# Performance work log

Hardware: AMD Instinct MI355X
Metric: run time of the kernel (lower is better)

## Reference

```python
import jax, jax.numpy as jnp
from jax import lax
import numpy as np

CHUNK = 64      # chunk_size init kwarg
MAX_LOG = 20.0  # clamp bound used in ssd()
DT_BIAS = 0.01
NEG_SLOPE = 0.01  # torch LeakyReLU default


def segsum(a):
    """a: (..., T) -> (..., T, T); ss[i,j] = sum_{k=j+1..i} a[k], -inf above diag."""
    T = a.shape[-1]
    rep = jnp.broadcast_to(a[..., :, None], a.shape + (T,))
    strict_lower = jnp.tril(jnp.ones((T, T), dtype=bool), -1)
    ss = jnp.cumsum(jnp.where(strict_lower, rep, 0.0), axis=-2)
    keep = jnp.tril(jnp.ones((T, T), dtype=bool), 0)
    return jnp.where(keep, ss, -jnp.inf)


def setup_inputs() -> dict:
    key = jax.random.key(0)
    ks = jax.random.split(key, 7)
    T, B, S, F = 4096, 4, 16, 64   # time, batch, spatial heads, in_channels
    N, P, K = 16, 64, 5            # state_dim, head_dim, conv_size
    CH = 2 * N + P + 1             # bc_conv out channels = 97
    return {
        "x": jax.random.normal(ks[0], (T, B, S, F), dtype=jnp.float32),
        "conv_w": jax.random.normal(ks[1], (CH, F, K), dtype=jnp.float32) * 0.05,
        "conv_b": jax.random.normal(ks[2], (CH,), dtype=jnp.float32) * 0.05,
        "pass_w": jax.random.normal(ks[3], (1, F), dtype=jnp.float32) * 0.1,
        "pass_b": jax.random.normal(ks[4], (1,), dtype=jnp.float32) * 0.1,
        "red_w": jax.random.normal(ks[5], (1, P), dtype=jnp.float32) * 0.1,
        "red_b": jax.random.normal(ks[6], (1,), dtype=jnp.float32) * 0.1,
        "dt_param": jnp.zeros((1,), dtype=jnp.float32),  # torch init [0.0]
    }


def _forward(x, conv_w, conv_b, pass_w, pass_b, red_w, red_b, dt_param):
    T, B, S, F = x.shape
    CH, _, K = conv_w.shape
    P = red_w.shape[1]
    N = (CH - P - 1) // 2
    c = T // CHUNK

    # ---- _compute_ssm_params (parallel mode, causal left-pad) ----
    xr = jnp.moveaxis(x.reshape(T, B * S, F), 0, 2)          # (bs, F, T)
    xp = jnp.pad(xr, ((0, 0), (0, 0), (K - 1, 0)))           # left pad context
    bcax = lax.conv_general_dilated(
        xp, conv_w, window_strides=(1,), padding="VALID",
        dimension_numbers=("NCH", "OIH", "NCH")) + conv_b[None, :, None]
    bcax = jax.nn.sigmoid(bcax) + bcax                        # (bs, CH, T)
    bcax = bcax.reshape(B, S, CH, T)
    Bm = bcax[:, :, :N, :]                                    # (b,s,n,t)
    Cm = bcax[:, :, N:2 * N, :]                               # (b,s,n,t)
    A = -jnp.abs(bcax[:, :, 2 * N, :])                        # (b,s,t)
    Xc = bcax[:, :, 2 * N + 1:, :]                            # (b,s,p,t)
    dt = jax.nn.softplus(dt_param)[0] + DT_BIAS
    lAd = dt * A                                              # (b,s,t)
    Bd = Bm * ((jnp.exp(lAd) - 1.0) / (A + 1e-9))[:, :, None, :]
    Dx = x @ pass_w[0] + pass_b[0]                            # (t,b,s) passthrough

    # ---- ssd: chunked Mamba-2 scan ----
    Xb = jnp.moveaxis(Xc, 3, 0).swapaxes(0, 1).reshape(B, c, CHUNK, S, P)
    Bb = jnp.moveaxis(Bd, 3, 0).swapaxes(0, 1).reshape(B, c, CHUNK, S, N)
    Cb = jnp.moveaxis(Cm, 3, 0).swapaxes(0, 1).reshape(B, c, CHUNK, S, N)
    Ab = lAd.reshape(B, S, c, CHUNK)                          # (b,s,c,l)
    A_cumsum = jnp.cumsum(Ab, axis=-1)                        # (b,s,c,l)

    L = jnp.exp(jnp.clip(segsum(Ab), -MAX_LOG, MAX_LOG))      # (b,s,c,l,l)
    Y_diag = jnp.einsum("bclsn,bcmsn,bsclm,bcmsp->bclsp", Cb, Bb, L, Xb)

    decay_states = jnp.exp(jnp.clip(A_cumsum[..., -1:] - A_cumsum, -MAX_LOG, MAX_LOG))
    states = jnp.einsum("bclsn,bscl,bclsp->bcspn", Bb, decay_states, Xb)
    states = jnp.concatenate([jnp.zeros_like(states[:, :1]), states], axis=1)

    A_last = jnp.pad(A_cumsum[..., -1], ((0, 0), (0, 0), (1, 0)))  # (b,s,c+1)
    decay_chunk = jnp.exp(jnp.clip(segsum(A_last), -MAX_LOG, MAX_LOG))
    new_states = jnp.einsum("bszc,bcspn->bzspn", decay_chunk, states)
    states_c = new_states[:, :-1]                             # (b,c,s,p,n)

    state_decay_out = jnp.exp(A_cumsum)                       # (b,s,c,l), no clamp (as in source)
    Y_off = jnp.einsum("bclsn,bcspn,bscl->bclsp", Cb, states_c, state_decay_out)

    Y = (Y_diag + Y_off).reshape(B, T, S, P).swapaxes(0, 1)   # (t,b,s,p)

    # ---- reduce + leaky-relu passthrough ----
    y = Y @ red_w[0] + red_b[0]                               # (t,b,s)
    return y + jnp.where(Dx >= 0, Dx, NEG_SLOPE * Dx)


def reference(x, conv_w, conv_b, pass_w, pass_b, red_w, red_b, dt_param):
    return _forward(x, conv_w, conv_b, pass_w, pass_b, red_w, red_b, dt_param)
```

## Files before the change

### kernel.cpp

```cpp
#include <hip/hip_runtime.h>
#include <hip/hip_bf16.h>
#include <math.h>


#define Tn 4096
#define BSn 64
#define Fn 64
#define CHn 97
#define CHP 112
#define Kn 5
#define Nn 16
#define NCn 64

typedef __attribute__((ext_vector_type(8))) short bf16x8;
typedef __attribute__((ext_vector_type(4))) float f32x4;

static __device__ __forceinline__ unsigned short f2bf(float v) {
    __hip_bfloat16 b = __float2bfloat16(v);
    return *reinterpret_cast<unsigned short*>(&b);
}
static __device__ __forceinline__ float bf2f(unsigned short u) {
    unsigned v = ((unsigned)u) << 16;
    return __builtin_bit_cast(float, v);
}

#define OFF_BD   0
#define OFF_CM   (OFF_BD + 4194304)
#define OFF_LAD  (OFF_CM + 4194304)
#define OFF_XQ   (OFF_LAD + 262144)
#define OFF_DL   (OFF_XQ + 262144)
#define OFF_ACS  (OFF_DL + 262144)
#define OFF_SRED (OFF_ACS + 262144)
#define OFF_CSUM (OFF_SRED + 65536)
#define OFF_SNS  (OFF_CSUM + 4096)
#define OFF_WBH  (OFF_SNS + 65536)
#define OFF_WBL  (OFF_WBH + 17920)

__global__ __launch_bounds__(256) void k_prep(const float* __restrict__ conv_w,
                                              const float* __restrict__ pass_w,
                                              unsigned short* __restrict__ wbh,
                                              unsigned short* __restrict__ wbl) {
    int idx = blockIdx.x * 256 + threadIdx.x;
    if (idx >= Kn * CHP * Fn) return;
    int f = idx & 63;
    int rest = idx >> 6;
    int ch = rest % CHP;
    int k = rest / CHP;
    float w = 0.f;
    if (ch < CHn) w = conv_w[(ch * Fn + f) * Kn + k];
    else if (ch == 97 && k == 4) w = pass_w[f];
    unsigned short hi = f2bf(w);
    wbh[idx] = hi;
    if (ch >= 32 && ch < 48)
        wbl[(k * 16 + (ch - 32)) * 64 + f] = f2bf(w - bf2f(hi));
}

__global__ __launch_bounds__(256) void k_conv(
    const float* __restrict__ x, const unsigned short* __restrict__ wbh,
    const unsigned short* __restrict__ wbl,
    const float* __restrict__ conv_b, const float* __restrict__ pass_b,
    const float* __restrict__ red_w, const float* __restrict__ red_b,
    const float* __restrict__ dtp,
    float* __restrict__ Bd_t, float* __restrict__ Cm_t,
    float* __restrict__ lAd_ws, float* __restrict__ xq_ws,
    float* __restrict__ DL_ws) {
    const int ci = blockIdx.x, bs = blockIdx.y;
    const int tid = threadIdx.x;
    const int wv = tid >> 6, lane = tid & 63;
    const int qd = lane >> 4, n = lane & 15;

    __shared__ alignas(16) unsigned short xsb[68 * 72];
    __shared__ alignas(16) unsigned short xlo[68 * 72];
    __shared__ float zsh[64];
    __shared__ float pxl[4][64];

    const int tB = (wv == 3) ? 6 : wv + 4;
    const unsigned short* pBw = (wv == 2) ? wbl : wbh;
    const int sB = (wv == 2) ? 16 : CHP;
    const int cB = (wv == 2) ? 0 : 16 * tB;
    bf16x8 wA[10], wB[10];
#pragma unroll
    for (int s = 0; s < 10; ++s) {
        const int k = s >> 1, f0 = 32 * (s & 1) + qd * 8;
        wA[s] = *(const bf16x8*)&wbh[((k * CHP + 16 * wv + n) << 6) + f0];
        wB[s] = *(const bf16x8*)&pBw[((k * sB + cB + n) << 6) + f0];
    }

    float4 v[5];
#pragma unroll
    for (int it = 0; it < 5; ++it) {
        int idx = tid + it * 256;
        int tt = idx >> 4, fq = (idx & 15) * 4;
        int t = ci * 64 - 4 + tt;
        v[it] = (idx < 68 * 16 && t >= 0)
                    ? *(const float4*)&x[(t * 64 + bs) * 64 + fq]
                    : make_float4(0.f, 0.f, 0.f, 0.f);
    }
#pragma unroll
    for (int it = 0; it < 5; ++it) {
        int idx = tid + it * 256;
        if (idx < 68 * 16) {
            int tt = idx >> 4, fq = (idx & 15) * 4;
            ushort4 h, lo;
            h.x = f2bf(v[it].x); lo.x = f2bf(v[it].x - bf2f(h.x));
            h.y = f2bf(v[it].y); lo.y = f2bf(v[it].y - bf2f(h.y));
            h.z = f2bf(v[it].z); lo.z = f2bf(v[it].z - bf2f(h.z));
            h.w = f2bf(v[it].w); lo.w = f2bf(v[it].w - bf2f(h.w));
            *(ushort4*)&xsb[tt * 72 + fq] = h;
            *(ushort4*)&xlo[tt * 72 + fq] = lo;
        }
    }
    __syncthreads();

    f32x4 accA[4], accB[4];
#pragma unroll
    for (int rg = 0; rg < 4; ++rg) {
        accA[rg] = (f32x4){0.f, 0.f, 0.f, 0.f};
        accB[rg] = (f32x4){0.f, 0.f, 0.f, 0.f};
    }
    if (wv == 2) {
#pragma unroll
        for (int s = 0; s < 10; ++s) {
            const int k = s >> 1, f0 = 32 * (s & 1) + qd * 8;
#pragma unroll
            for (int rg = 0; rg < 4; ++rg) {
                bf16x8 av = *(const bf16x8*)&xsb[(16 * rg + n + k) * 72 + f0];
                bf16x8 al = *(const bf16x8*)&xlo[(16 * rg + n + k) * 72 + f0];
                accA[rg] = __builtin_amdgcn_mfma_f32_16x16x32_bf16(av, wA[s], accA[rg], 0, 0, 0);
                accA[rg] = __builtin_amdgcn_mfma_f32_16x16x32_bf16(al, wA[s], accA[rg], 0, 0, 0);
                accA[rg] = __builtin_amdgcn_mfma_f32_16x16x32_bf16(av, wB[s], accA[rg], 0, 0, 0);
            }
        }
    } else {
#pragma unroll
        for (int s = 0; s < 10; ++s) {
            const int k = s >> 1, f0 = 32 * (s & 1) + qd * 8;
#pragma unroll
            for (int rg = 0; rg < 4; ++rg) {
                bf16x8 av = *(const bf16x8*)&xsb[(16 * rg + n + k) * 72 + f0];
                accA[rg] = __builtin_amdgcn_mfma_f32_16x16x32_bf16(av, wA[s], accA[rg], 0, 0, 0);
                accB[rg] = __builtin_amdgcn_mfma_f32_16x16x32_bf16(av, wB[s], accB[rg], 0, 0, 0);
            }
        }
    }

    const int cbase = (bs * 64 + ci) * 64;
    float px[4][4];
#pragma unroll
    for (int rg = 0; rg < 4; ++rg)
#pragma unroll
        for (int reg = 0; reg < 4; ++reg) px[rg][reg] = 0.f;

    if (wv == 0) {
        const float cb4 = conv_b[64 + n], rw4 = red_w[31 + n];
#pragma unroll
        for (int rg = 0; rg < 4; ++rg)
#pragma unroll
            for (int reg = 0; reg < 4; ++reg) {
                float z = accB[rg][reg] + cb4;
                px[rg][reg] = (z + 1.f / (1.f + __expf(-z))) * rw4;
            }
    } else if (wv == 1) {
        const float cb1 = conv_b[16 + n];
        const float cb5 = conv_b[80 + n], rw5 = red_w[47 + n];
#pragma unroll
        for (int rg = 0; rg < 4; ++rg)
#pragma unroll
            for (int reg = 0; reg < 4; ++reg) {
                float z1 = accA[rg][reg] + cb1;
                Cm_t[(cbase + 16 * rg + 4 * qd + reg) * 16 + n] =
                    z1 + 1.f / (1.f + __expf(-z1));
                float z5 = accB[rg][reg] + cb5;
                px[rg][reg] = (z5 + 1.f / (1.f + __expf(-z5))) * rw5;
            }
    } else if (wv == 2) {
        const float cb2 = conv_b[32 + n];
        const float rw2 = (n >= 1) ? red_w[n - 1] : 0.f;
#pragma unroll
        for (int rg = 0; rg < 4; ++rg)
#pragma unroll
            for (int reg = 0; reg < 4; ++reg) {
                if (n == 0) zsh[16 * rg + 4 * qd + reg] = accA[rg][reg];
                float z = accA[rg][reg] + cb2;
                px[rg][reg] = (z + 1.f / (1.f + __expf(-z))) * rw2;
            }
    } else {
        const float cb3 = conv_b[48 + n], rw3 = red_w[15 + n];
        const float cb6 = conv_b[96], rw6 = red_w[63];
        const float pb = pass_b[0], rb = red_b[0];
#pragma unroll
        for (int rg = 0; rg < 4; ++rg)
#pragma unroll
            for (int reg = 0; reg < 4; ++reg) {
                float z3 = accA[rg][reg] + cb3;
                px[rg][reg] = (z3 + 1.f / (1.f + __expf(-z3))) * rw3;
                if (n == 0) {
                    float z6 = accB[rg][reg] + cb6;
                    px[rg][reg] += (z6 + 1.f / (1.f + __expf(-z6))) * rw6;
                }
                if (n == 1) {
                    float Dx = accB[rg][reg] + pb;
                    float DL = (Dx >= 0.f) ? Dx : 0.01f * Dx;
                    DL_ws[bs * Tn + ci * 64 + 16 * rg + 4 * qd + reg] = DL + rb;
                }
            }
    }

#pragma unroll
    for (int m = 1; m < 16; m <<= 1)
#pragma unroll
        for (int rg = 0; rg < 4; ++rg)
#pragma unroll
            for (int reg = 0; reg < 4; ++reg)
                px[rg][reg] += __shfl_xor(px[rg][reg], m, 64);
    if (n == 0)
#pragma unroll
        for (int rg = 0; rg < 4; ++rg)
#pragma unroll
            for (int reg = 0; reg < 4; ++reg)
                pxl[wv][16 * rg + 4 * qd + reg] = px[rg][reg];
    __syncthreads();

    if (wv == 0) {
        const float dt = log1pf(expf(dtp[0])) + 0.01f;
        float zA = zsh[lane] + conv_b[32];
        float aA = zA + 1.f / (1.f + __expf(-zA));
        float An = -fabsf(aA);
        float lAd = dt * An;
        lAd_ws[bs * Tn + ci * 64 + lane] = lAd;
        float fl = (__expf(lAd) - 1.f) / (An + 1e-9f);
        const float cb0 = conv_b[n];
#pragma unroll
        for (int rg = 0; rg < 4; ++rg)
#pragma unroll
            for (int reg = 0; reg < 4; ++reg) {
                float z = accA[rg][reg] + cb0;
                float a = z + 1.f / (1.f + __expf(-z));
                float fr = __shfl(fl, 16 * rg + 4 * qd + reg, 64);
                Bd_t[(cbase + 16 * rg + 4 * qd + reg) * 16 + n] = a * fr;
            }
    } else if (wv == 1) {
        xq_ws[bs * Tn + ci * 64 + lane] =
            pxl[0][lane] + pxl[1][lane] + pxl[2][lane] + pxl[3][lane];
    }
}

__global__ __launch_bounds__(256) void k_chunk(
    const float* __restrict__ lAd_ws, const float* __restrict__ xq_ws,
    const float* __restrict__ Bd_t, float* __restrict__ Acs_ws,
    float* __restrict__ sred_ws, float* __restrict__ csum_ws) {
    const int bs = blockIdx.y;
    const int tid = threadIdx.x, wv = tid >> 6, l = tid & 63;
    const int ci = blockIdx.x * 4 + wv;
    __shared__ float aL[4][64], acs[4][64], vv[4][64];
    __shared__ float Bt[4][64 * 17], part[4][4][16];
    const int base = bs * Tn + ci * 64;

    aL[wv][l] = lAd_ws[base + l];
    const float4* brow = (const float4*)&Bd_t[((bs * 64 + ci) * 64 + l) * 16];
    float4 b0 = brow[0], b1 = brow[1], b2 = brow[2], b3 = brow[3];
    float* bt = &Bt[wv][l * 17];
    bt[0] = b0.x;  bt[1] = b0.y;  bt[2] = b0.z;  bt[3] = b0.w;
    bt[4] = b1.x;  bt[5] = b1.y;  bt[6] = b1.z;  bt[7] = b1.w;
    bt[8] = b2.x;  bt[9] = b2.y;  bt[10] = b2.z; bt[11] = b2.w;
    bt[12] = b3.x; bt[13] = b3.y; bt[14] = b3.z; bt[15] = b3.w;
    __syncthreads();

    float s = 0.f;
    for (int k2 = 0; k2 < 64; ++k2) {
        float a = aL[wv][k2];
        if (k2 <= l) s += a;
    }
    acs[wv][l] = s;
    Acs_ws[base + l] = s;
    __syncthreads();

    float tot = acs[wv][63];
    float ds = __expf(fmaxf(tot - s, -20.f));
    vv[wv][l] = ds * xq_ws[base + l];
    __syncthreads();

    int nn = l & 15, q = l >> 4;
    float p = 0.f;
#pragma unroll
    for (int i = 0; i < 16; ++i)
        p += Bt[wv][(q * 16 + i) * 17 + nn] * vv[wv][q * 16 + i];
    part[wv][q][nn] = p;
    __syncthreads();
    if (l < 16)
        sred_ws[(bs * 64 + ci) * 16 + l] =
            part[wv][0][l] + part[wv][1][l] + part[wv][2][l] + part[wv][3][l];
    if (l == 0) csum_ws[bs * 64 + ci] = tot;
}

__global__ __launch_bounds__(256) void k_scan(const float* __restrict__ sred_ws,
                                              const float* __restrict__ csum_ws,
                                              float* __restrict__ sns_ws) {
    const int wid = blockIdx.x * 4 + (threadIdx.x >> 6);
    const int ci = threadIdx.x & 63;
    const int bs = wid >> 4, n = wid & 15;
    float s = sred_ws[(bs * 64 + ci) * 16 + n];
    float d = __expf(csum_ws[bs * 64 + ci]);
#pragma unroll
    for (int k = 1; k < 64; k <<= 1) {
        float dp = __shfl_up(d, k, 64);
        float sp = __shfl_up(s, k, 64);
        if (ci >= k) {
            s = d * sp + s;
            d = d * dp;
        }
    }
    float se = __shfl_up(s, 1, 64);
    sns_ws[(bs * 64 + ci) * 16 + n] = (ci == 0) ? 0.f : se;
}

__global__ __launch_bounds__(256) void k_y(
    const float* __restrict__ Cm_t, const float* __restrict__ Bd_t,
    const float* __restrict__ xq_ws, const float* __restrict__ Acs_ws,
    const float* __restrict__ sns_ws, const float* __restrict__ DL_ws,
    float* __restrict__ out) {
    const int bs = blockIdx.y;
    const int tid = threadIdx.x;
    const int wv = tid >> 6, l = tid & 63;
    const int ci = blockIdx.x * 4 + wv;
    __shared__ float Bt[4][64 * 17], xv[4][64], ac[4][64], sn[4][16];
    const int base = bs * Tn + ci * 64;

    xv[wv][l] = xq_ws[base + l];
    ac[wv][l] = Acs_ws[base + l];
    if (l < 16) sn[wv][l] = sns_ws[(bs * 64 + ci) * 16 + l];
    const float4* brow = (const float4*)&Bd_t[((bs * 64 + ci) * 64 + l) * 16];
    float4 b0 = brow[0], b1 = brow[1], b2 = brow[2], b3 = brow[3];
    float* bt = &Bt[wv][l * 17];
    bt[0] = b0.x;  bt[1] = b0.y;  bt[2] = b0.z;  bt[3] = b0.w;
    bt[4] = b1.x;  bt[5] = b1.y;  bt[6] = b1.z;  bt[7] = b1.w;
    bt[8] = b2.x;  bt[9] = b2.y;  bt[10] = b2.z; bt[11] = b2.w;
    bt[12] = b3.x; bt[13] = b3.y; bt[14] = b3.z; bt[15] = b3.w;
    const float4* crow = (const float4*)&Cm_t[((bs * 64 + ci) * 64 + l) * 16];
    float4 c0 = crow[0], c1 = crow[1], c2 = crow[2], c3 = crow[3];
    __syncthreads();

    const float acl = ac[wv][l];
    float y = 0.f;
    for (int m = 0; m < 64; ++m) {
        const float* br = &Bt[wv][m * 17];
        float g = c0.x * br[0] + c0.y * br[1] + c0.z * br[2] + c0.w * br[3] +
                  c1.x * br[4] + c1.y * br[5] + c1.z * br[6] + c1.w * br[7] +
                  c2.x * br[8] + c2.y * br[9] + c2.z * br[10] + c2.w * br[11] +
                  c3.x * br[12] + c3.y * br[13] + c3.z * br[14] + c3.w * br[15];
        float arg = (m <= l) ? fmaxf(acl - ac[wv][m], -20.f) : -20.f;
        y += __expf(arg) * g * xv[wv][m];
    }
    const float* s = sn[wv];
    float go = c0.x * s[0] + c0.y * s[1] + c0.z * s[2] + c0.w * s[3] +
               c1.x * s[4] + c1.y * s[5] + c1.z * s[6] + c1.w * s[7] +
               c2.x * s[8] + c2.y * s[9] + c2.z * s[10] + c2.w * s[11] +
               c3.x * s[12] + c3.y * s[13] + c3.z * s[14] + c3.w * s[15];
    y += __expf(acl) * go;

    out[(ci * 64 + l) * 64 + bs] = y + DL_ws[base + l];
}

extern "C" void kernel_launch(void* const* d_in, const int* in_sizes, int n_in,
                              void* d_out, int out_size, void* d_ws,
                              size_t ws_size, hipStream_t stream) {
    const float* x = (const float*)d_in[0];
    const float* conv_w = (const float*)d_in[1];
    const float* conv_b = (const float*)d_in[2];
    const float* pass_w = (const float*)d_in[3];
    const float* pass_b = (const float*)d_in[4];
    const float* red_w = (const float*)d_in[5];
    const float* red_b = (const float*)d_in[6];
    const float* dtp = (const float*)d_in[7];
    float* out = (float*)d_out;
    float* W = (float*)d_ws;
    (void)in_sizes; (void)n_in; (void)out_size; (void)ws_size;

    float* Bd_t = W + OFF_BD;
    float* Cm_t = W + OFF_CM;
    float* lAd_ws = W + OFF_LAD;
    float* xq_ws = W + OFF_XQ;
    float* DL_ws = W + OFF_DL;
    float* Acs_ws = W + OFF_ACS;
    float* sred_ws = W + OFF_SRED;
    float* csum_ws = W + OFF_CSUM;
    float* sns_ws = W + OFF_SNS;
    unsigned short* wbh = (unsigned short*)(W + OFF_WBH);
    unsigned short* wbl = (unsigned short*)(W + OFF_WBL);

    k_prep<<<dim3((Kn * CHP * Fn + 255) / 256), dim3(256), 0, stream>>>(
        conv_w, pass_w, wbh, wbl);
    k_conv<<<dim3(NCn, BSn), dim3(256), 0, stream>>>(
        x, wbh, wbl, conv_b, pass_b, red_w, red_b, dtp,
        Bd_t, Cm_t, lAd_ws, xq_ws, DL_ws);
    k_chunk<<<dim3(NCn / 4, BSn), dim3(256), 0, stream>>>(
        lAd_ws, xq_ws, Bd_t, Acs_ws, sred_ws, csum_ws);
    k_scan<<<dim3(256), dim3(256), 0, stream>>>(sred_ws, csum_ws, sns_ws);
    k_y<<<dim3(NCn / 4, BSn), dim3(256), 0, stream>>>(
        Cm_t, Bd_t, xq_ws, Acs_ws, sns_ws, DL_ws, out);
}
```

Before: 200.3 us.

## Fuse chunk-local state and diagonal output into conv kernel, drop Bd round-trip

Merges the chunk-local work (within-chunk cumsum of log decay, chunk state reduction, and intra-chunk diagonal output) into the conv kernel. B, C and the per-chunk scalars stay in a reused shared-memory pool instead of going to global memory and being re-read by two later kernels. The final kernel now only adds the inter-chunk state contribution to a precomputed partial output. This removes one launch and the Bd_t/lAd/xq/DL global traffic, at the cost of a longer conv kernel with extra barriers and more per-block LDS and register pressure.

```diff
diff --git a/kernel.cpp b/kernel.cpp
--- a/kernel.cpp
+++ b/kernel.cpp
@@ -55,24 +55,29 @@
         wbl[(k * 16 + (ch - 32)) * 64 + f] = f2bf(w - bf2f(hi));
 }
 
-__global__ __launch_bounds__(256) void k_conv(
+__global__ __launch_bounds__(256) void k_fwd(
     const float* __restrict__ x, const unsigned short* __restrict__ wbh,
     const unsigned short* __restrict__ wbl,
     const float* __restrict__ conv_b, const float* __restrict__ pass_b,
     const float* __restrict__ red_w, const float* __restrict__ red_b,
     const float* __restrict__ dtp,
-    float* __restrict__ Bd_t, float* __restrict__ Cm_t,
-    float* __restrict__ lAd_ws, float* __restrict__ xq_ws,
-    float* __restrict__ DL_ws) {
+    float* __restrict__ Cm_t, float* __restrict__ Acs_ws,
+    float* __restrict__ yp_ws, float* __restrict__ sred_ws,
+    float* __restrict__ csum_ws) {
     const int ci = blockIdx.x, bs = blockIdx.y;
     const int tid = threadIdx.x;
     const int wv = tid >> 6, lane = tid & 63;
     const int qd = lane >> 4, n = lane & 15;
 
-    __shared__ alignas(16) unsigned short xsb[68 * 72];
-    __shared__ alignas(16) unsigned short xlo[68 * 72];
-    __shared__ float zsh[64];
-    __shared__ float pxl[4][64];
+    __shared__ alignas(16) unsigned char pool[19584];
+    unsigned short* xsb = (unsigned short*)pool;
+    unsigned short* xlo = (unsigned short*)(pool + 9792);
+    float* B0  = (float*)pool;
+    float* Ct  = (float*)(pool + 5120);
+    float* pxl = (float*)(pool + 10240);
+    float* px2 = (float*)(pool + 11264);
+    float* zsh = (float*)(pool + 12288);
+    float* dl  = (float*)(pool + 12544);
 
     const int tB = (wv == 3) ? 6 : wv + 4;
     const unsigned short* pBw = (wv == 2) ? wbl : wbh;
@@ -143,6 +148,7 @@
             }
         }
     }
+    __syncthreads();
 
     const int cbase = (bs * 64 + ci) * 64;
     float px[4][4];
@@ -152,13 +158,19 @@
         for (int reg = 0; reg < 4; ++reg) px[rg][reg] = 0.f;
 
     if (wv == 0) {
+        const float cb0 = conv_b[n];
         const float cb4 = conv_b[64 + n], rw4 = red_w[31 + n];
 #pragma unroll
         for (int rg = 0; rg < 4; ++rg)
 #pragma unroll
             for (int reg = 0; reg < 4; ++reg) {
-                float z = accB[rg][reg] + cb4;
-                px[rg][reg] = (z + 1.f / (1.f + __expf(-z))) * rw4;
+                int row = 16 * rg + 4 * qd + reg;
+                float z0 = accA[rg][reg] + cb0;
+                float a0 = z0 + 1.f / (1.f + __expf(-z0));
+                accA[rg][reg] = a0;
+                B0[row * 20 + n] = a0;
+                float z4 = accB[rg][reg] + cb4;
+                px[rg][reg] = (z4 + 1.f / (1.f + __expf(-z4))) * rw4;
             }
     } else if (wv == 1) {
         const float cb1 = conv_b[16 + n];
@@ -167,9 +179,11 @@
         for (int rg = 0; rg < 4; ++rg)
 #pragma unroll
             for (int reg = 0; reg < 4; ++reg) {
+                int row = 16 * rg + 4 * qd + reg;
                 float z1 = accA[rg][reg] + cb1;
-                Cm_t[(cbase + 16 * rg + 4 * qd + reg) * 16 + n] =
-                    z1 + 1.f / (1.f + __expf(-z1));
+                float a1 = z1 + 1.f / (1.f + __expf(-z1));
+                Ct[row * 20 + n] = a1;
+                Cm_t[(cbase + row) * 16 + n] = a1;
                 float z5 = accB[rg][reg] + cb5;
                 px[rg][reg] = (z5 + 1.f / (1.f + __expf(-z5))) * rw5;
             }
@@ -180,7 +194,8 @@
         for (int rg = 0; rg < 4; ++rg)
 #pragma unroll
             for (int reg = 0; reg < 4; ++reg) {
-                if (n == 0) zsh[16 * rg + 4 * qd + reg] = accA[rg][reg];
+                int row = 16 * rg + 4 * qd + reg;
+                if (n == 0) zsh[row] = accA[rg][reg];
                 float z = accA[rg][reg] + cb2;
                 px[rg][reg] = (z + 1.f / (1.f + __expf(-z))) * rw2;
             }
@@ -192,6 +207,7 @@
         for (int rg = 0; rg < 4; ++rg)
 #pragma unroll
             for (int reg = 0; reg < 4; ++reg) {
+                int row = 16 * rg + 4 * qd + reg;
                 float z3 = accA[rg][reg] + cb3;
                 px[rg][reg] = (z3 + 1.f / (1.f + __expf(-z3))) * rw3;
                 if (n == 0) {
@@ -201,11 +217,10 @@
                 if (n == 1) {
                     float Dx = accB[rg][reg] + pb;
                     float DL = (Dx >= 0.f) ? Dx : 0.01f * Dx;
-                    DL_ws[bs * Tn + ci * 64 + 16 * rg + 4 * qd + reg] = DL + rb;
+                    dl[row] = DL + rb;
                 }
             }
     }
-
 #pragma unroll
     for (int m = 1; m < 16; m <<= 1)
 #pragma unroll
@@ -218,79 +233,71 @@
         for (int rg = 0; rg < 4; ++rg)
 #pragma unroll
             for (int reg = 0; reg < 4; ++reg)
-                pxl[wv][16 * rg + 4 * qd + reg] = px[rg][reg];
-    __syncthreads();
+                pxl[wv * 64 + 16 * rg + 4 * qd + reg] = px[rg][reg];
+    __syncthreads();
+
+    const int l = lane;
+    const float dt = log1pf(expf(dtp[0])) + 0.01f;
+    float zA = zsh[l] + conv_b[32];
+    float aA = zA + 1.f / (1.f + __expf(-zA));
+    float An = -fabsf(aA);
+    float lAd = dt * An;
+    float fac = (__expf(lAd) - 1.f) / (An + 1e-9f);
+    float s = lAd;
+#pragma unroll
+    for (int k = 1; k < 64; k <<= 1) {
+        float t = __shfl_up(s, k, 64);
+        if (l >= k) s += t;
+    }
+    const float acs_l = s;
+    const float tot = __shfl(s, 63, 64);
+    float xq = pxl[0 * 64 + l] + pxl[1 * 64 + l] + pxl[2 * 64 + l] + pxl[3 * 64 + l];
+    const float wd = fac * xq;
+    const float wsd = wd * __expf(fmaxf(tot - acs_l, -20.f));
+    if (wv == 3) {
+        Acs_ws[bs * Tn + ci * 64 + l] = acs_l;
+        if (l == 0) csum_ws[bs * 64 + ci] = tot;
+    }
+
+    const float4 cc0 = *(const float4*)&Ct[l * 20 + 0];
+    const float4 cc1 = *(const float4*)&Ct[l * 20 + 4];
+    const float4 cc2 = *(const float4*)&Ct[l * 20 + 8];
+    const float4 cc3 = *(const float4*)&Ct[l * 20 + 12];
+    float part = 0.f;
+#pragma unroll
+    for (int mm = 0; mm < 16; ++mm) {
+        const int m = 16 * wv + mm;
+        const float4 b0 = *(const float4*)&B0[m * 20 + 0];
+        const float4 b1 = *(const float4*)&B0[m * 20 + 4];
+        const float4 b2 = *(const float4*)&B0[m * 20 + 8];
+        const float4 b3 = *(const float4*)&B0[m * 20 + 12];
+        float g = cc0.x * b0.x + cc0.y * b0.y + cc0.z * b0.z + cc0.w * b0.w +
+                  cc1.x * b1.x + cc1.y * b1.y + cc1.z * b1.z + cc1.w * b1.w +
+                  cc2.x * b2.x + cc2.y * b2.y + cc2.z * b2.z + cc2.w * b2.w +
+                  cc3.x * b3.x + cc3.y * b3.y + cc3.z * b3.z + cc3.w * b3.w;
+        float am = __shfl(acs_l, m, 64);
+        float wm = __shfl(wd, m, 64);
+        float arg = (m <= l) ? fmaxf(acs_l - am, -20.f) : -20.f;
+        part += __expf(arg) * g * wm;
+    }
+    px2[wv * 64 + l] = part;
 
     if (wv == 0) {
-        const float dt = log1pf(expf(dtp[0])) + 0.01f;
-        float zA = zsh[lane] + conv_b[32];
-        float aA = zA + 1.f / (1.f + __expf(-zA));
-        float An = -fabsf(aA);
-        float lAd = dt * An;
-        lAd_ws[bs * Tn + ci * 64 + lane] = lAd;
-        float fl = (__expf(lAd) - 1.f) / (An + 1e-9f);
-        const float cb0 = conv_b[n];
-#pragma unroll
-        for (int rg = 0; rg < 4; ++rg)
-#pragma unroll
-            for (int reg = 0; reg < 4; ++reg) {
-                float z = accA[rg][reg] + cb0;
-                float a = z + 1.f / (1.f + __expf(-z));
-                float fr = __shfl(fl, 16 * rg + 4 * qd + reg, 64);
-                Bd_t[(cbase + 16 * rg + 4 * qd + reg) * 16 + n] = a * fr;
-            }
-    } else if (wv == 1) {
-        xq_ws[bs * Tn + ci * 64 + lane] =
-            pxl[0][lane] + pxl[1][lane] + pxl[2][lane] + pxl[3][lane];
-    }
-}
-
-__global__ __launch_bounds__(256) void k_chunk(
-    const float* __restrict__ lAd_ws, const float* __restrict__ xq_ws,
-    const float* __restrict__ Bd_t, float* __restrict__ Acs_ws,
-    float* __restrict__ sred_ws, float* __restrict__ csum_ws) {
-    const int bs = blockIdx.y;
-    const int tid = threadIdx.x, wv = tid >> 6, l = tid & 63;
-    const int ci = blockIdx.x * 4 + wv;
-    __shared__ float aL[4][64], acs[4][64], vv[4][64];
-    __shared__ float Bt[4][64 * 17], part[4][4][16];
-    const int base = bs * Tn + ci * 64;
-
-    aL[wv][l] = lAd_ws[base + l];
-    const float4* brow = (const float4*)&Bd_t[((bs * 64 + ci) * 64 + l) * 16];
-    float4 b0 = brow[0], b1 = brow[1], b2 = brow[2], b3 = brow[3];
-    float* bt = &Bt[wv][l * 17];
-    bt[0] = b0.x;  bt[1] = b0.y;  bt[2] = b0.z;  bt[3] = b0.w;
-    bt[4] = b1.x;  bt[5] = b1.y;  bt[6] = b1.z;  bt[7] = b1.w;
-    bt[8] = b2.x;  bt[9] = b2.y;  bt[10] = b2.z; bt[11] = b2.w;
-    bt[12] = b3.x; bt[13] = b3.y; bt[14] = b3.z; bt[15] = b3.w;
-    __syncthreads();
-
-    float s = 0.f;
-    for (int k2 = 0; k2 < 64; ++k2) {
-        float a = aL[wv][k2];
-        if (k2 <= l) s += a;
-    }
-    acs[wv][l] = s;
-    Acs_ws[base + l] = s;
-    __syncthreads();
-
-    float tot = acs[wv][63];
-    float ds = __expf(fmaxf(tot - s, -20.f));
-    vv[wv][l] = ds * xq_ws[base + l];
-    __syncthreads();
-
-    int nn = l & 15, q = l >> 4;
-    float p = 0.f;
-#pragma unroll
-    for (int i = 0; i < 16; ++i)
-        p += Bt[wv][(q * 16 + i) * 17 + nn] * vv[wv][q * 16 + i];
-    part[wv][q][nn] = p;
-    __syncthreads();
-    if (l < 16)
-        sred_ws[(bs * 64 + ci) * 16 + l] =
-            part[wv][0][l] + part[wv][1][l] + part[wv][2][l] + part[wv][3][l];
-    if (l == 0) csum_ws[bs * 64 + ci] = tot;
+        float sp = 0.f;
+#pragma unroll
+        for (int rg = 0; rg < 4; ++rg)
+#pragma unroll
+            for (int reg = 0; reg < 4; ++reg)
+                sp += accA[rg][reg] * __shfl(wsd, 16 * rg + 4 * qd + reg, 64);
+        sp += __shfl_xor(sp, 16, 64);
+        sp += __shfl_xor(sp, 32, 64);
+        if (l < 16) sred_ws[(bs * 64 + ci) * 16 + l] = sp;
+    }
+    __syncthreads();
+
+    if (wv == 0)
+        yp_ws[bs * Tn + ci * 64 + l] =
+            px2[0 * 64 + l] + px2[1 * 64 + l] + px2[2 * 64 + l] + px2[3 * 64 + l] + dl[l];
 }
 
 __global__ __launch_bounds__(256) void k_scan(const float* __restrict__ sred_ws,
@@ -314,51 +321,30 @@
     sns_ws[(bs * 64 + ci) * 16 + n] = (ci == 0) ? 0.f : se;
 }
 
-__global__ __launch_bounds__(256) void k_y(
-    const float* __restrict__ Cm_t, const float* __restrict__ Bd_t,
-    const float* __restrict__ xq_ws, const float* __restrict__ Acs_ws,
-    const float* __restrict__ sns_ws, const float* __restrict__ DL_ws,
+__global__ __launch_bounds__(256) void k_out(
+    const float* __restrict__ Cm_t, const float* __restrict__ Acs_ws,
+    const float* __restrict__ sns_ws, const float* __restrict__ yp_ws,
     float* __restrict__ out) {
     const int bs = blockIdx.y;
     const int tid = threadIdx.x;
     const int wv = tid >> 6, l = tid & 63;
     const int ci = blockIdx.x * 4 + wv;
-    __shared__ float Bt[4][64 * 17], xv[4][64], ac[4][64], sn[4][16];
+    __shared__ float sn[4][16];
     const int base = bs * Tn + ci * 64;
 
-    xv[wv][l] = xq_ws[base + l];
-    ac[wv][l] = Acs_ws[base + l];
     if (l < 16) sn[wv][l] = sns_ws[(bs * 64 + ci) * 16 + l];
-    const float4* brow = (const float4*)&Bd_t[((bs * 64 + ci) * 64 + l) * 16];
-    float4 b0 = brow[0], b1 = brow[1], b2 = brow[2], b3 = brow[3];
-    float* bt = &Bt[wv][l * 17];
-    bt[0] = b0.x;  bt[1] = b0.y;  bt[2] = b0.z;  bt[3] = b0.w;
-    bt[4] = b1.x;  bt[5] = b1.y;  bt[6] = b1.z;  bt[7] = b1.w;
-    bt[8] = b2.x;  bt[9] = b2.y;  bt[10] = b2.z; bt[11] = b2.w;
-    bt[12] = b3.x; bt[13] = b3.y; bt[14] = b3.z; bt[15] = b3.w;
     const float4* crow = (const float4*)&Cm_t[((bs * 64 + ci) * 64 + l) * 16];
     float4 c0 = crow[0], c1 = crow[1], c2 = crow[2], c3 = crow[3];
-    __syncthreads();
-
-    const float acl = ac[wv][l];
-    float y = 0.f;
-    for (int m = 0; m < 64; ++m) {
-        const float* br = &Bt[wv][m * 17];
-        float g = c0.x * br[0] + c0.y * br[1] + c0.z * br[2] + c0.w * br[3] +
-                  c1.x * br[4] + c1.y * br[5] + c1.z * br[6] + c1.w * br[7] +
-                  c2.x * br[8] + c2.y * br[9] + c2.z * br[10] + c2.w * br[11] +
-                  c3.x * br[12] + c3.y * br[13] + c3.z * br[14] + c3.w * br[15];
-        float arg = (m <= l) ? fmaxf(acl - ac[wv][m], -20.f) : -20.f;
-        y += __expf(arg) * g * xv[wv][m];
-    }
+    float yp = yp_ws[base + l];
+    float acl = Acs_ws[base + l];
+    __syncthreads();
+
     const float* s = sn[wv];
     float go = c0.x * s[0] + c0.y * s[1] + c0.z * s[2] + c0.w * s[3] +
                c1.x * s[4] + c1.y * s[5] + c1.z * s[6] + c1.w * s[7] +
                c2.x * s[8] + c2.y * s[9] + c2.z * s[10] + c2.w * s[11] +
                c3.x * s[12] + c3.y * s[13] + c3.z * s[14] + c3.w * s[15];
-    y += __expf(acl) * go;
-
-    out[(ci * 64 + l) * 64 + bs] = y + DL_ws[base + l];
+    out[(ci * 64 + l) * 64 + bs] = yp + __expf(acl) * go;
 }
 
 extern "C" void kernel_launch(void* const* d_in, const int* in_sizes, int n_in,
@@ -376,11 +362,8 @@
     float* W = (float*)d_ws;
     (void)in_sizes; (void)n_in; (void)out_size; (void)ws_size;
 
-    float* Bd_t = W + OFF_BD;
     float* Cm_t = W + OFF_CM;
-    float* lAd_ws = W + OFF_LAD;
-    float* xq_ws = W + OFF_XQ;
-    float* DL_ws = W + OFF_DL;
+    float* yp_ws = W + OFF_DL;
     float* Acs_ws = W + OFF_ACS;
     float* sred_ws = W + OFF_SRED;
     float* csum_ws = W + OFF_CSUM;
@@ -390,12 +373,10 @@
 
     k_prep<<<dim3((Kn * CHP * Fn + 255) / 256), dim3(256), 0, stream>>>(
         conv_w, pass_w, wbh, wbl);
-    k_conv<<<dim3(NCn, BSn), dim3(256), 0, stream>>>(
+    k_fwd<<<dim3(NCn, BSn), dim3(256), 0, stream>>>(
         x, wbh, wbl, conv_b, pass_b, red_w, red_b, dtp,
-        Bd_t, Cm_t, lAd_ws, xq_ws, DL_ws);
-    k_chunk<<<dim3(NCn / 4, BSn), dim3(256), 0, stream>>>(
-        lAd_ws, xq_ws, Bd_t, Acs_ws, sred_ws, csum_ws);
+        Cm_t, Acs_ws, yp_ws, sred_ws, csum_ws);
     k_scan<<<dim3(256), dim3(256), 0, stream>>>(sred_ws, csum_ws, sns_ws);
-    k_y<<<dim3(NCn / 4, BSn), dim3(256), 0, stream>>>(
-        Cm_t, Bd_t, xq_ws, Acs_ws, sns_ws, DL_ws, out);
-}
+    k_out<<<dim3(NCn / 4, BSn), dim3(256), 0, stream>>>(
+        Cm_t, Acs_ws, sns_ws, yp_ws, out);
+}
```

After: 203.6 us. No clear change (+1.6%).
